# Optimization experiments

Measured on AMD Instinct MI355X. Metric: run time of the kernel, lower is better.

## Reference

```python
import jax, jax.numpy as jnp
import numpy as np

B, C4, H, W = 2, 128, 128, 128
POOL_SIZE = 10


def setup_inputs() -> dict:
    key = jax.random.key(0)
    k1, k2, k3 = jax.random.split(key, 3)
    feature = jax.random.normal(k1, (B, C4, H, W), dtype=jnp.float32)
    K = H * W
    # valid boxes: x1<x2, y1<y2, inside the feature map
    xy1 = jax.random.uniform(k2, (B, K, 2), dtype=jnp.float32) * jnp.array([W * 0.5, H * 0.5], jnp.float32)
    wh = jax.random.uniform(k3, (B, K, 2), dtype=jnp.float32) * jnp.array([W * 0.45, H * 0.45], jnp.float32) + 1.0
    boxes = jnp.concatenate([xy1, xy1 + wh], axis=-1)  # [B, K, 4] = (x1,y1,x2,y2)
    return {"feature": feature, "boxes": boxes, "pool_size": POOL_SIZE}


def reference(feature, boxes, pool_size):
    # feature: [B, 4*C, H, W]; boxes: [B, K, 4]; output: [B, C, K, 4]
    Bn, C4n, Hn, Wn = feature.shape
    C = C4n // 4
    K = boxes.shape[1]
    P = pool_size + 1
    x1, y1, x2, y2 = (boxes[..., i] for i in range(4))  # each [B, K]
    t = jnp.arange(P, dtype=feature.dtype) / pool_size  # [P]
    sx = x1[..., None] + t * (x2 - x1)[..., None]  # [B, K, P] along-x samples
    sy = y1[..., None] + t * (y2 - y1)[..., None]  # [B, K, P] along-y samples
    cx1 = jnp.broadcast_to(x1[..., None], sx.shape)
    cx2 = jnp.broadcast_to(x2[..., None], sx.shape)
    cy1 = jnp.broadcast_to(y1[..., None], sy.shape)
    cy2 = jnp.broadcast_to(y2[..., None], sy.shape)
    # border order: 0=top (y=y1), 1=left (x=x1), 2=bottom (y=y2), 3=right (x=x2)
    xs = jnp.stack([sx, cx1, sx, cx2], axis=1)  # [B, 4, K, P]
    ys = jnp.stack([cy1, sy, cy2, sy], axis=1)  # [B, 4, K, P]

    valid = (xs > -1.0) & (xs < Wn) & (ys > -1.0) & (ys < Hn)
    x = jnp.clip(xs, 0.0, Wn - 1)
    y = jnp.clip(ys, 0.0, Hn - 1)
    x0 = jnp.floor(x).astype(jnp.int32)
    y0 = jnp.floor(y).astype(jnp.int32)
    x1i = jnp.minimum(x0 + 1, Wn - 1)
    y1i = jnp.minimum(y0 + 1, Hn - 1)
    lx = (x - x0)[:, :, None]  # [B, 4, 1, K, P]
    ly = (y - y0)[:, :, None]

    featf = feature.reshape(Bn, 4, C, Hn * Wn)  # channel group g feeds border g

    def gather(yi, xi):
        idx = (yi * Wn + xi).reshape(Bn, 4, 1, K * P)
        return jnp.take_along_axis(featf, idx, axis=3).reshape(Bn, 4, C, K, P)

    val = (gather(y0, x0) * (1 - ly) * (1 - lx)
           + gather(y0, x1i) * (1 - ly) * lx
           + gather(y1i, x0) * ly * (1 - lx)
           + gather(y1i, x1i) * ly * lx)
    val = jnp.where(valid[:, :, None], val, 0.0)
    out = val.max(axis=-1)  # max-pool over the P samples per border -> [B, 4, C, K]
    return out.transpose(0, 2, 3, 1)  # [B, C, K, 4]
```

## Files before the change

kernel.cpp:

```cpp
#include <hip/hip_runtime.h>
#include <math.h>

#define BN   2
#define CG   32
#define HH   128
#define WW   128
#define HWSZ (HH*WW)
#define KK   16384
#define CAP  512
#define CHUNK 128
#define NCHK (CAP / CHUNK)
#define SLICES 128
#define SLICE_BOXES (KK / SLICES)

#define WS_F16_OFF   (0u)
#define WS_TMP_OFF   (8u << 20)
#define WS_BKT_OFF   (16u << 20)
#define WS_PCNT_OFF  (24u << 20)
#define WS_PBASE_OFF ((24u << 20) + (512u<<10))
#define WS_CNT_OFF   ((24u << 20) + (1024u<<10))
#define WS_NEED      ((24u << 20) + (1028u<<10))

typedef float vf4 __attribute__((ext_vector_type(4)));
typedef _Float16 h8 __attribute__((ext_vector_type(8)));

__device__ inline unsigned int pack_h2(float a, float b) {
  unsigned short ua = __builtin_bit_cast(unsigned short, (_Float16)a);
  unsigned short ub = __builtin_bit_cast(unsigned short, (_Float16)b);
  return (unsigned int)ua | ((unsigned int)ub << 16);
}

__global__ __launch_bounds__(256) void transpose_f16_kernel(
    const float* __restrict__ feat, unsigned short* __restrict__ ws) {
  __shared__ uint2 lds[128 * 9];
  const int blk = blockIdx.x;
  const int s  = blk & 7;
  const int i0 = (blk >> 3) * 128;
  const int t  = threadIdx.x;

  const int iL = (t & 31) * 4;
  const int cq = t >> 5;

  const float* src = feat + (size_t)s * (CG * HWSZ) + i0 + iL;
  vf4 r[4];
#pragma unroll
  for (int cc = 0; cc < 4; ++cc)
    r[cc] = *(const vf4*)(src + (size_t)(cq * 4 + cc) * HWSZ);

#pragma unroll
  for (int ii = 0; ii < 4; ++ii) {
    uint2 q;
    q.x = pack_h2(r[0][ii], r[1][ii]);
    q.y = pack_h2(r[2][ii], r[3][ii]);
    lds[(iL + ii) * 9 + cq] = q;
  }
  __syncthreads();

  uint2* dst = (uint2*)(ws + ((size_t)s * HWSZ + i0) * CG);
  const int q2 = t & 7;
  const int ih = t >> 3;
#pragma unroll
  for (int it = 0; it < 4; ++it) {
    const int i = ih + 32 * it;
    dst[i * 8 + q2] = lds[i * 9 + q2];
  }
}

__global__ __launch_bounds__(128) void bin_count_kernel(
    const float* __restrict__ boxes, unsigned int* __restrict__ pcnt) {
  __shared__ unsigned int hist[512];
  const int blk = blockIdx.x;
  const int b  = blk >> 7;
  const int sl = blk & 127;
  const int t  = threadIdx.x;
#pragma unroll
  for (int i = 0; i < 4; ++i) hist[t + 128 * i] = 0u;
  __syncthreads();

  const vf4 bx = *(const vf4*)(boxes + ((size_t)b * KK + sl * SLICE_BOXES + t) * 4);
#pragma unroll
  for (int g = 0; g < 4; ++g) {
    const float fix = (g == 0) ? bx[1] : (g == 1) ? bx[0]
                     : (g == 2) ? bx[3] : bx[2];
    const int f0 = (int)fminf(fmaxf(fix, 0.0f), 127.0f);
    atomicAdd(&hist[(g << 7) | f0], 1u);
  }
  __syncthreads();
#pragma unroll
  for (int i = 0; i < 4; ++i)
    pcnt[sl * 1024 + b * 512 + t + 128 * i] = hist[t + 128 * i];
}

__global__ __launch_bounds__(256) void bin_scan_kernel(
    const unsigned int* __restrict__ pcnt, unsigned int* __restrict__ pbase,
    unsigned int* __restrict__ cnt) {
  const int gbin = blockIdx.x * 256 + threadIdx.x;
  unsigned int base = 0u;
#pragma unroll 8
  for (int sl = 0; sl < SLICES; ++sl) {
    pbase[sl * 1024 + gbin] = base;
    base += pcnt[sl * 1024 + gbin];
  }
  cnt[gbin] = base;
}

__global__ __launch_bounds__(128) void bin_scatter_kernel(
    const float* __restrict__ boxes, const unsigned int* __restrict__ pbase,
    uint4* __restrict__ bkt) {
  __shared__ unsigned int hist[512];
  const int blk = blockIdx.x;
  const int b  = blk >> 7;
  const int sl = blk & 127;
  const int t  = threadIdx.x;
#pragma unroll
  for (int i = 0; i < 4; ++i) hist[t + 128 * i] = 0u;
  __syncthreads();

  const int k = sl * SLICE_BOXES + t;
  const vf4 bx = *(const vf4*)(boxes + ((size_t)b * KK + k) * 4);
#pragma unroll
  for (int g = 0; g < 4; ++g) {
    const bool horiz = (g & 1) == 0;
    const float fix = (g == 0) ? bx[1] : (g == 1) ? bx[0]
                     : (g == 2) ? bx[3] : bx[2];
    const float fc = fminf(fmaxf(fix, 0.0f), 127.0f);
    const int f0 = (int)fc;
    const unsigned int rank = atomicAdd(&hist[(g << 7) | f0], 1u);
    const int gbin = b * 512 + (g << 7) + f0;
    const unsigned int slot = pbase[sl * 1024 + gbin] + rank;
    if (slot < CAP) {
      const float mov_s = horiz ? bx[0] : bx[1];
      const float mov_d = horiz ? (bx[2] - bx[0]) : (bx[3] - bx[1]);
      const float lf    = fc - (float)f0;
      const bool  fok   = (fix > -1.0f) && (fix < 128.0f);
      uint4 rec;
      rec.x = __builtin_bit_cast(unsigned int, mov_s);
      rec.y = __builtin_bit_cast(unsigned int, mov_d);
      rec.z = __builtin_bit_cast(unsigned int, lf);
      rec.w = (unsigned int)k | (fok ? 0x80000000u : 0u);
      bkt[(size_t)gbin * CAP + slot] = rec;
    }
  }
}

__global__ __launch_bounds__(256) void border_gather_binned(
    const unsigned short* __restrict__ wsu,
    const unsigned int* __restrict__ cnt, const uint4* __restrict__ bkt,
    const int* __restrict__ psp, unsigned short* __restrict__ tmp) {
  __shared__ _Float16 tile[2 * 128 * 32];
  __shared__ float stf[64];

  const int blk  = blockIdx.x;
  const int s    = blk & 7;
  const int f0   = (blk >> 3) & 127;
  const int ch   = blk >> 10;
  const int g    = s & 3;
  const int b    = s >> 2;
  const int gbin = s * 128 + f0;
  const int n    = min((int)cnt[gbin], CAP);
  const int i0   = ch * CHUNK;
  const int i1   = min(n, i0 + CHUNK);
  if (i1 <= i0) return;

  const int t  = threadIdx.x;
  const int ps = *psp;
  if (t < 64) stf[t] = (float)(t <= ps ? t : ps) / (float)ps;

  const bool horiz = (g & 1) == 0;
  const int f1 = min(f0 + 1, 127);
  const _Float16* slab = (const _Float16*)wsu + (size_t)s * (HWSZ * CG);

#pragma unroll
  for (int it = 0; it < 4; ++it) {
    const int chunk = it * 256 + t;
    const int cc   = chunk >> 9;
    const int rem  = chunk & 511;
    const int p    = rem >> 2;
    const int slot = rem & 3;
    const int fcc  = cc ? f1 : f0;
    const size_t srci = horiz ? ((size_t)(fcc * 128 + p) * 32)
                              : ((size_t)(p * 128 + fcc) * 32);
    const uint4 v = *(const uint4*)(slab + srci + slot * 8);
    const int slotS = slot ^ ((p >> 1) & 3);
    *(uint4*)((char*)tile + cc * 8192 + p * 64 + slotS * 16) = v;
  }
  __syncthreads();

  const int w      = t >> 6;
  const int oct    = t & 3;
  const int slot16 = (t >> 2) & 15;

  for (int base = i0 + w * 16; base < i1; base += 64) {
    const int ii  = base + slot16;
    const bool vb = ii < i1;
    const int iic = vb ? ii : i0;
    const uint4 rec = bkt[(size_t)gbin * CAP + iic];
    const float mov_s = __builtin_bit_cast(float, rec.x);
    const float mov_d = __builtin_bit_cast(float, rec.y);
    const float lf    = __builtin_bit_cast(float, rec.z);
    const bool  fok   = (rec.w >> 31) != 0u;
    const int   kid   = (int)(rec.w & 0xFFFFu);

    h8 acc = (h8)(_Float16)(-65504.0f);

#define SAMPLE(TP) do {                                                    \
      const float mov = fmaf((TP), mov_d, mov_s);                          \
      const bool ok = fok && (mov > -1.0f) && (mov < 128.0f);              \
      const float mc = fminf(fmaxf(mov, 0.0f), 127.0f);                    \
      const int m0 = (int)mc;                                              \
      const float lm = mc - (float)m0;                                     \
      const int m1 = min(m0 + 1, 127);                                     \
      const int a0 = (m0 << 6) + ((oct ^ ((m0 >> 1) & 3)) << 4);           \
      const int a1 = (m1 << 6) + ((oct ^ ((m1 >> 1) & 3)) << 4);           \
      const h8 f00 = *(const h8*)((const char*)tile + a0);                 \
      const h8 f01 = *(const h8*)((const char*)tile + a1);                 \
      const h8 f10 = *(const h8*)((const char*)tile + 8192 + a0);          \
      const h8 f11 = *(const h8*)((const char*)tile + 8192 + a1);          \
      const _Float16 w00 = (_Float16)((1.0f - lf) * (1.0f - lm));          \
      const _Float16 w01 = (_Float16)((1.0f - lf) * lm);                   \
      const _Float16 w10 = (_Float16)(lf * (1.0f - lm));                   \
      const _Float16 w11 = (_Float16)(lf * lm);                            \
      h8 v = f00 * w00 + f01 * w01 + f10 * w10 + f11 * w11;                \
      v = ok ? v : (h8)(_Float16)0.0f;                                     \
      acc = __builtin_elementwise_max(acc, v);                             \
    } while (0)

    if (ps == 10) {
#pragma unroll
      for (int p = 0; p <= 10; ++p) SAMPLE((float)p / 10.0f);
    } else {
      for (int p = 0; p <= ps; ++p) SAMPLE(stf[p]);
    }
#undef SAMPLE

    if (vb) {
      h8* dst = (h8*)(tmp + ((size_t)(b * 4 + g) * KK + kid) * 32 + oct * 8);
      *dst = acc;
    }
  }
}

__global__ __launch_bounds__(256) void untranspose_kernel(
    const unsigned short* __restrict__ tmp, float* __restrict__ out) {
  __shared__ float lds[4 * 32 * 33];
  const int blk = blockIdx.x;
  const int b   = blk >> 9;
  const int k0  = (blk & 511) * 32;
  const int t   = threadIdx.x;

#pragma unroll
  for (int it = 0; it < 2; ++it) {
    const int chunk = it * 256 + t;
    const int g   = chunk >> 7;
    const int rem = chunk & 127;
    const int kk  = rem >> 2;
    const int co8 = rem & 3;
    const h8 v = *(const h8*)((const _Float16*)tmp
                 + ((size_t)(b * 4 + g) * KK + k0 + kk) * 32 + co8 * 8);
#pragma unroll
    for (int j = 0; j < 8; ++j)
      lds[g * (32 * 33) + kk * 33 + co8 * 8 + j] = (float)v[j];
  }
  __syncthreads();

#pragma unroll
  for (int it = 0; it < 4; ++it) {
    const int chunk = it * 256 + t;
    const int c  = chunk >> 5;
    const int kk = chunk & 31;
    vf4 v;
#pragma unroll
    for (int g = 0; g < 4; ++g)
      v[g] = lds[g * (32 * 33) + kk * 33 + c];
    vf4* dst = (vf4*)(out + ((size_t)(b * CG + c) * KK + k0 + kk) * 4);
    __builtin_nontemporal_store(v, dst);
  }
}

__global__ __launch_bounds__(128) void border_align_fallback(
    const float* __restrict__ base, const float* __restrict__ boxes,
    const int* __restrict__ psp, float* __restrict__ out) {
  const int blk = blockIdx.x;
  const int b = blk >> 10;
  const int t = threadIdx.x;
  const int g = t >> 5, c = t & 31;
  const int k0 = (blk & 1023) * 16;
  const int ps = *psp;
  const float psf = (float)ps;
  const float* slab = base + (size_t)(b * 4 + g) * (CG * HWSZ) + (size_t)c * HWSZ;
  for (int kk = 0; kk < 16; ++kk) {
    const int kbox = k0 + kk;
    const float x1 = boxes[((size_t)b * KK + kbox) * 4 + 0];
    const float y1 = boxes[((size_t)b * KK + kbox) * 4 + 1];
    const float x2 = boxes[((size_t)b * KK + kbox) * 4 + 2];
    const float y2 = boxes[((size_t)b * KK + kbox) * 4 + 3];
    float m = -INFINITY;
    for (int p = 0; p <= ps; ++p) {
      const float tf = (float)p / psf;
      float x, y;
      if      (g == 0) { x = x1 + tf * (x2 - x1); y = y1; }
      else if (g == 1) { x = x1; y = y1 + tf * (y2 - y1); }
      else if (g == 2) { x = x1 + tf * (x2 - x1); y = y2; }
      else             { x = x2; y = y1 + tf * (y2 - y1); }
      const bool valid = (x > -1.0f) && (x < 128.0f) && (y > -1.0f) && (y < 128.0f);
      const float xc = fminf(fmaxf(x, 0.0f), 127.0f);
      const float yc = fminf(fmaxf(y, 0.0f), 127.0f);
      const int x0 = (int)xc, y0 = (int)yc;
      const float lx = xc - (float)x0, ly = yc - (float)y0;
      const int x1i = min(x0 + 1, 127), y1i = min(y0 + 1, 127);
      const float f00 = slab[y0 * WW + x0],  f01 = slab[y0 * WW + x1i];
      const float f10 = slab[y1i * WW + x0], f11 = slab[y1i * WW + x1i];
      float v = f00 * (1 - ly) * (1 - lx) + f01 * (1 - ly) * lx
              + f10 * ly * (1 - lx) + f11 * ly * lx;
      v = valid ? v : 0.0f;
      m = fmaxf(m, v);
    }
    out[(((size_t)(b * CG + c)) * KK + kbox) * 4 + g] = m;
  }
}

extern "C" void kernel_launch(void* const* d_in, const int* in_sizes, int n_in,
                              void* d_out, int out_size, void* d_ws, size_t ws_size,
                              hipStream_t stream) {
  const float* feature = (const float*)d_in[0];
  const float* boxes   = (const float*)d_in[1];
  const int*   psp     = (const int*)d_in[2];
  float*       out     = (float*)d_out;

  if (ws_size >= WS_NEED) {
    char* ws = (char*)d_ws;
    unsigned short* wsf16 = (unsigned short*)(ws + WS_F16_OFF);
    unsigned short* tmp   = (unsigned short*)(ws + WS_TMP_OFF);
    uint4*          bkt   = (uint4*)(ws + WS_BKT_OFF);
    unsigned int*   pcnt  = (unsigned int*)(ws + WS_PCNT_OFF);
    unsigned int*   pbase = (unsigned int*)(ws + WS_PBASE_OFF);
    unsigned int*   cnt   = (unsigned int*)(ws + WS_CNT_OFF);

    hipLaunchKernelGGL(transpose_f16_kernel, dim3(8 * (HWSZ / 128)),
                       dim3(256), 0, stream, feature, wsf16);
    hipLaunchKernelGGL(bin_count_kernel, dim3(BN * SLICES), dim3(128), 0,
                       stream, boxes, pcnt);
    hipLaunchKernelGGL(bin_scan_kernel, dim3(4), dim3(256), 0, stream,
                       pcnt, pbase, cnt);
    hipLaunchKernelGGL(bin_scatter_kernel, dim3(BN * SLICES), dim3(128), 0,
                       stream, boxes, pbase, bkt);
    hipLaunchKernelGGL(border_gather_binned, dim3(NCHK * 1024), dim3(256), 0,
                       stream, wsf16, cnt, bkt, psp, tmp);
    hipLaunchKernelGGL(untranspose_kernel, dim3(BN * 512), dim3(256), 0, stream,
                       tmp, out);
  } else {
    hipLaunchKernelGGL(border_align_fallback, dim3(BN * (KK / 16)), dim3(128), 0,
                       stream, feature, boxes, psp, out);
  }
}
```

Before: 107.7 us.

## Fuse atomic bucket sort into transpose kernel and drop the count/scan passes

Replaces the three-kernel count, scan and scatter binning pipeline with one atomic-based bucket sort. Each of 64 blocks builds a local histogram in shared memory, then reserves a base offset per bin with one global atomicAdd on a padded counter array. These sort blocks run in the same grid as the FP16 feature transpose blocks, and a small kernel zeroes the counters first. The aim is to cut kernel launches and the per-slice prefix arrays; in exchange, record order within a bucket becomes nondeterministic, which the max reduction tolerates. The gather chunk size is also doubled from 128 to 256, so fewer gather blocks handle more records each.

Result: faster. 96.32 us (-10.5%).

```diff
diff --git a/kernel.cpp b/kernel.cpp
--- a/kernel.cpp
+++ b/kernel.cpp
@@ -8,18 +8,16 @@
 #define HWSZ (HH*WW)
 #define KK   16384
 #define CAP  512
-#define CHUNK 128
+#define CHUNK 256
 #define NCHK (CAP / CHUNK)
-#define SLICES 128
-#define SLICE_BOXES (KK / SLICES)
+#define SORTB 64
+#define BOX_PER_SORTB (BN * KK / SORTB)
 
 #define WS_F16_OFF   (0u)
 #define WS_TMP_OFF   (8u << 20)
 #define WS_BKT_OFF   (16u << 20)
-#define WS_PCNT_OFF  (24u << 20)
-#define WS_PBASE_OFF ((24u << 20) + (512u<<10))
-#define WS_CNT_OFF   ((24u << 20) + (1024u<<10))
-#define WS_NEED      ((24u << 20) + (1028u<<10))
+#define WS_CNT_OFF   (24u << 20)
+#define WS_NEED      ((24u << 20) + (64u << 10))
 
 typedef float vf4 __attribute__((ext_vector_type(4)));
 typedef _Float16 h8 __attribute__((ext_vector_type(8)));
@@ -30,115 +28,108 @@
   return (unsigned int)ua | ((unsigned int)ub << 16);
 }
 
-__global__ __launch_bounds__(256) void transpose_f16_kernel(
-    const float* __restrict__ feat, unsigned short* __restrict__ ws) {
-  __shared__ uint2 lds[128 * 9];
+__global__ __launch_bounds__(256) void zero_cnt_kernel(unsigned int* __restrict__ cnt) {
+  cnt[blockIdx.x * 256 + threadIdx.x] = 0u;
+}
+
+__global__ __launch_bounds__(256) void sort_transpose_kernel(
+    const float* __restrict__ feat, unsigned short* __restrict__ ws,
+    const float* __restrict__ boxes, unsigned int* __restrict__ cnt,
+    uint4* __restrict__ bkt) {
+  __shared__ char smem[128 * 9 * 8];
   const int blk = blockIdx.x;
-  const int s  = blk & 7;
-  const int i0 = (blk >> 3) * 128;
-  const int t  = threadIdx.x;
-
-  const int iL = (t & 31) * 4;
-  const int cq = t >> 5;
-
-  const float* src = feat + (size_t)s * (CG * HWSZ) + i0 + iL;
-  vf4 r[4];
-#pragma unroll
-  for (int cc = 0; cc < 4; ++cc)
-    r[cc] = *(const vf4*)(src + (size_t)(cq * 4 + cc) * HWSZ);
-
-#pragma unroll
-  for (int ii = 0; ii < 4; ++ii) {
-    uint2 q;
-    q.x = pack_h2(r[0][ii], r[1][ii]);
-    q.y = pack_h2(r[2][ii], r[3][ii]);
-    lds[(iL + ii) * 9 + cq] = q;
-  }
-  __syncthreads();
-
-  uint2* dst = (uint2*)(ws + ((size_t)s * HWSZ + i0) * CG);
-  const int q2 = t & 7;
-  const int ih = t >> 3;
-#pragma unroll
-  for (int it = 0; it < 4; ++it) {
-    const int i = ih + 32 * it;
-    dst[i * 8 + q2] = lds[i * 9 + q2];
-  }
-}
-
-__global__ __launch_bounds__(128) void bin_count_kernel(
-    const float* __restrict__ boxes, unsigned int* __restrict__ pcnt) {
-  __shared__ unsigned int hist[512];
-  const int blk = blockIdx.x;
-  const int b  = blk >> 7;
-  const int sl = blk & 127;
-  const int t  = threadIdx.x;
-#pragma unroll
-  for (int i = 0; i < 4; ++i) hist[t + 128 * i] = 0u;
-  __syncthreads();
-
-  const vf4 bx = *(const vf4*)(boxes + ((size_t)b * KK + sl * SLICE_BOXES + t) * 4);
-#pragma unroll
-  for (int g = 0; g < 4; ++g) {
-    const float fix = (g == 0) ? bx[1] : (g == 1) ? bx[0]
-                     : (g == 2) ? bx[3] : bx[2];
-    const int f0 = (int)fminf(fmaxf(fix, 0.0f), 127.0f);
-    atomicAdd(&hist[(g << 7) | f0], 1u);
-  }
-  __syncthreads();
-#pragma unroll
-  for (int i = 0; i < 4; ++i)
-    pcnt[sl * 1024 + b * 512 + t + 128 * i] = hist[t + 128 * i];
-}
-
-__global__ __launch_bounds__(256) void bin_scan_kernel(
-    const unsigned int* __restrict__ pcnt, unsigned int* __restrict__ pbase,
-    unsigned int* __restrict__ cnt) {
-  const int gbin = blockIdx.x * 256 + threadIdx.x;
-  unsigned int base = 0u;
-#pragma unroll 8
-  for (int sl = 0; sl < SLICES; ++sl) {
-    pbase[sl * 1024 + gbin] = base;
-    base += pcnt[sl * 1024 + gbin];
-  }
-  cnt[gbin] = base;
-}
-
-__global__ __launch_bounds__(128) void bin_scatter_kernel(
-    const float* __restrict__ boxes, const unsigned int* __restrict__ pbase,
-    uint4* __restrict__ bkt) {
-  __shared__ unsigned int hist[512];
-  const int blk = blockIdx.x;
-  const int b  = blk >> 7;
-  const int sl = blk & 127;
-  const int t  = threadIdx.x;
-#pragma unroll
-  for (int i = 0; i < 4; ++i) hist[t + 128 * i] = 0u;
-  __syncthreads();
-
-  const int k = sl * SLICE_BOXES + t;
-  const vf4 bx = *(const vf4*)(boxes + ((size_t)b * KK + k) * 4);
-#pragma unroll
-  for (int g = 0; g < 4; ++g) {
-    const bool horiz = (g & 1) == 0;
-    const float fix = (g == 0) ? bx[1] : (g == 1) ? bx[0]
-                     : (g == 2) ? bx[3] : bx[2];
-    const float fc = fminf(fmaxf(fix, 0.0f), 127.0f);
-    const int f0 = (int)fc;
-    const unsigned int rank = atomicAdd(&hist[(g << 7) | f0], 1u);
-    const int gbin = b * 512 + (g << 7) + f0;
-    const unsigned int slot = pbase[sl * 1024 + gbin] + rank;
-    if (slot < CAP) {
-      const float mov_s = horiz ? bx[0] : bx[1];
-      const float mov_d = horiz ? (bx[2] - bx[0]) : (bx[3] - bx[1]);
-      const float lf    = fc - (float)f0;
-      const bool  fok   = (fix > -1.0f) && (fix < 128.0f);
-      uint4 rec;
-      rec.x = __builtin_bit_cast(unsigned int, mov_s);
-      rec.y = __builtin_bit_cast(unsigned int, mov_d);
-      rec.z = __builtin_bit_cast(unsigned int, lf);
-      rec.w = (unsigned int)k | (fok ? 0x80000000u : 0u);
-      bkt[(size_t)gbin * CAP + slot] = rec;
+  const int t   = threadIdx.x;
+
+  if (blk < SORTB) {
+    unsigned int* hist = (unsigned int*)smem;
+    unsigned int* basE = (unsigned int*)smem + 512;
+    const int batch = blk >> 5;
+    const int k0    = (blk & 31) * BOX_PER_SORTB;
+    hist[t] = 0u; hist[t + 256] = 0u;
+    __syncthreads();
+
+    vf4 bx[2];
+    unsigned short rnk[2][4];
+    int bin[2][4];
+#pragma unroll
+    for (int i = 0; i < 2; ++i) {
+      const int k = k0 + i * 256 + t;
+      bx[i] = *(const vf4*)(boxes + ((size_t)batch * KK + k) * 4);
+#pragma unroll
+      for (int g = 0; g < 4; ++g) {
+        const float fix = (g == 0) ? bx[i][1] : (g == 1) ? bx[i][0]
+                         : (g == 2) ? bx[i][3] : bx[i][2];
+        const int f0 = (int)fminf(fmaxf(fix, 0.0f), 127.0f);
+        bin[i][g] = (g << 7) | f0;
+        rnk[i][g] = (unsigned short)atomicAdd(&hist[bin[i][g]], 1u);
+      }
+    }
+    __syncthreads();
+
+#pragma unroll
+    for (int j = 0; j < 2; ++j) {
+      const int idx = j * 256 + t;
+      const unsigned int c = hist[idx];
+      basE[idx] = c ? atomicAdd(&cnt[(size_t)((batch << 9) + idx) * 16], c) : 0u;
+    }
+    __syncthreads();
+
+#pragma unroll
+    for (int i = 0; i < 2; ++i) {
+      const int k = k0 + i * 256 + t;
+#pragma unroll
+      for (int g = 0; g < 4; ++g) {
+        const bool horiz = (g & 1) == 0;
+        const float fix = (g == 0) ? bx[i][1] : (g == 1) ? bx[i][0]
+                         : (g == 2) ? bx[i][3] : bx[i][2];
+        const float fc = fminf(fmaxf(fix, 0.0f), 127.0f);
+        const int f0 = bin[i][g] & 127;
+        const unsigned int slot = basE[bin[i][g]] + rnk[i][g];
+        if (slot < CAP) {
+          const float mov_s = horiz ? bx[i][0] : bx[i][1];
+          const float mov_d = horiz ? (bx[i][2] - bx[i][0]) : (bx[i][3] - bx[i][1]);
+          const float lf    = fc - (float)f0;
+          const bool  fok   = (fix > -1.0f) && (fix < 128.0f);
+          uint4 rec;
+          rec.x = __builtin_bit_cast(unsigned int, mov_s);
+          rec.y = __builtin_bit_cast(unsigned int, mov_d);
+          rec.z = __builtin_bit_cast(unsigned int, lf);
+          rec.w = (unsigned int)k | (fok ? 0x80000000u : 0u);
+          bkt[(size_t)((batch << 9) + bin[i][g]) * CAP + slot] = rec;
+        }
+      }
+    }
+  } else {
+    uint2* lds = (uint2*)smem;
+    const int idx = blk - SORTB;
+    const int s  = idx & 7;
+    const int i0 = (idx >> 3) * 128;
+
+    const int iL = (t & 31) * 4;
+    const int cq = t >> 5;
+
+    const float* src = feat + (size_t)s * (CG * HWSZ) + i0 + iL;
+    vf4 r[4];
+#pragma unroll
+    for (int cc = 0; cc < 4; ++cc)
+      r[cc] = *(const vf4*)(src + (size_t)(cq * 4 + cc) * HWSZ);
+
+#pragma unroll
+    for (int ii = 0; ii < 4; ++ii) {
+      uint2 q;
+      q.x = pack_h2(r[0][ii], r[1][ii]);
+      q.y = pack_h2(r[2][ii], r[3][ii]);
+      lds[(iL + ii) * 9 + cq] = q;
+    }
+    __syncthreads();
+
+    uint2* dst = (uint2*)(ws + ((size_t)s * HWSZ + i0) * CG);
+    const int q2 = t & 7;
+    const int ih = t >> 3;
+#pragma unroll
+    for (int it = 0; it < 4; ++it) {
+      const int i = ih + 32 * it;
+      dst[i * 8 + q2] = lds[i * 9 + q2];
     }
   }
 }
@@ -157,7 +148,7 @@
   const int g    = s & 3;
   const int b    = s >> 2;
   const int gbin = s * 128 + f0;
-  const int n    = min((int)cnt[gbin], CAP);
+  const int n    = min((int)cnt[(size_t)gbin * 16], CAP);
   const int i0   = ch * CHUNK;
   const int i1   = min(n, i0 + CHUNK);
   if (i1 <= i0) return;
@@ -332,18 +323,11 @@
     unsigned short* wsf16 = (unsigned short*)(ws + WS_F16_OFF);
     unsigned short* tmp   = (unsigned short*)(ws + WS_TMP_OFF);
     uint4*          bkt   = (uint4*)(ws + WS_BKT_OFF);
-    unsigned int*   pcnt  = (unsigned int*)(ws + WS_PCNT_OFF);
-    unsigned int*   pbase = (unsigned int*)(ws + WS_PBASE_OFF);
     unsigned int*   cnt   = (unsigned int*)(ws + WS_CNT_OFF);
 
-    hipLaunchKernelGGL(transpose_f16_kernel, dim3(8 * (HWSZ / 128)),
-                       dim3(256), 0, stream, feature, wsf16);
-    hipLaunchKernelGGL(bin_count_kernel, dim3(BN * SLICES), dim3(128), 0,
-                       stream, boxes, pcnt);
-    hipLaunchKernelGGL(bin_scan_kernel, dim3(4), dim3(256), 0, stream,
-                       pcnt, pbase, cnt);
-    hipLaunchKernelGGL(bin_scatter_kernel, dim3(BN * SLICES), dim3(128), 0,
-                       stream, boxes, pbase, bkt);
+    hipLaunchKernelGGL(zero_cnt_kernel, dim3(64), dim3(256), 0, stream, cnt);
+    hipLaunchKernelGGL(sort_transpose_kernel, dim3(SORTB + 8 * (HWSZ / 128)),
+                       dim3(256), 0, stream, feature, wsf16, boxes, cnt, bkt);
     hipLaunchKernelGGL(border_gather_binned, dim3(NCHK * 1024), dim3(256), 0,
                        stream, wsf16, cnt, bkt, psp, tmp);
     hipLaunchKernelGGL(untranspose_kernel, dim3(BN * 512), dim3(256), 0, stream,
```
